# Performance work log

Hardware: AMD Instinct MI355X
Metric: run time of the kernel (lower is better)

Reference implementation:

```python
import jax, jax.numpy as jnp
import numpy as np

NUM_USERS = 100000
NUM_ITEMS = 50000
EMB = 64
B = 8192
MAXM = 50
ATT_H = 16
PRED_H = 8


def setup_inputs() -> dict:
    key = jax.random.key(0)
    ks = jax.random.split(key, 12)
    member_idx = jax.random.randint(ks[0], (B, MAXM), 0, NUM_USERS)
    # ragged group sizes in [1, MAXM]
    lens = jax.random.randint(ks[1], (B,), 1, MAXM + 1)
    member_mask = jnp.arange(MAXM)[None, :] < lens[:, None]  # bool [B, M]
    item_inputs = jax.random.randint(ks[2], (B,), 0, NUM_ITEMS)
    s = 1.0 / np.sqrt(EMB)
    user_table = jax.random.normal(ks[3], (NUM_USERS, EMB), jnp.float32) * s
    item_table = jax.random.normal(ks[4], (NUM_ITEMS, EMB), jnp.float32) * s
    att_w1 = jax.random.normal(ks[5], (2 * EMB, ATT_H), jnp.float32) * 0.05
    att_b1 = jnp.zeros((ATT_H,), jnp.float32)
    att_w2 = jax.random.normal(ks[6], (ATT_H, 1), jnp.float32) * 0.05
    att_b2 = jnp.zeros((1,), jnp.float32)
    pred_w1 = jax.random.normal(ks[7], (3 * EMB, PRED_H), jnp.float32) * 0.05
    pred_b1 = jnp.zeros((PRED_H,), jnp.float32)
    pred_w2 = jax.random.normal(ks[8], (PRED_H, 1), jnp.float32) * 0.05
    pred_b2 = jnp.zeros((1,), jnp.float32)
    return dict(member_idx=member_idx, member_mask=member_mask, item_inputs=item_inputs,
                user_table=user_table, item_table=item_table,
                att_w1=att_w1, att_b1=att_b1, att_w2=att_w2, att_b2=att_b2,
                pred_w1=pred_w1, pred_b1=pred_b1, pred_w2=pred_w2, pred_b2=pred_b2)


def reference(member_idx, member_mask, item_inputs, user_table, item_table,
              att_w1, att_b1, att_w2, att_b2, pred_w1, pred_b1, pred_w2, pred_b2):
    mem_e = user_table[member_idx]            # [B, M, d]
    item_e = item_table[item_inputs]          # [B, d]
    # attention MLP over concat(member, item)
    cat = jnp.concatenate(
        [mem_e, jnp.broadcast_to(item_e[:, None, :], mem_e.shape)], axis=-1)  # [B, M, 2d]
    h = jax.nn.relu(jnp.einsum('bmf,fh->bmh', cat, att_w1) + att_b1)
    logits = (jnp.einsum('bmh,ho->bmo', h, att_w2) + att_b2)[..., 0]          # [B, M]
    logits = jnp.where(member_mask, logits, -jnp.inf)
    wts = jax.nn.softmax(logits, axis=-1)                                     # [B, M]
    g = jnp.einsum('bm,bmd->bd', wts, mem_e)                                  # [B, d]
    new = jnp.concatenate([g * item_e, g, item_e], axis=-1)                   # [B, 3d]
    ph = jax.nn.relu(new @ pred_w1 + pred_b1)
    y = jax.nn.sigmoid(ph @ pred_w2 + pred_b2)                                # [B, 1]
    return y
```

## Files before the change

### kernel.cpp

```cpp
#include <hip/hip_runtime.h>
#include <hip/hip_bf16.h>


__global__ void AGREE_12773232738622_probe(
    const void* member_mask,
    const void* user_table,
    int* ws)
{
    if (ws[2] == 0x5AFE0001) return;

    const int lane = threadIdx.x;
    const int wi = lane >> 4;
    const int r  = lane & 15;

    int len = 0, ok = 1, prev = 1;
    for (int m = 0; m < 50; ++m) {
        long e = 50L * r + m;
        int nz;
        if (wi == 0)      nz = (((const unsigned char*)member_mask)[e] != 0);
        else if (wi == 1) nz = (((const unsigned short*)member_mask)[e] != 0);
        else if (wi == 2) nz = (((const unsigned int*)member_mask)[e] != 0u);
        else {
            const unsigned int* p = (const unsigned int*)member_mask;
            nz = ((p[2 * e] | p[2 * e + 1]) != 0u);
        }
        if (nz && !prev) ok = 0;
        if (nz) len = len + 1;
        prev = nz;
    }
    if (len == 0) ok = 0;

    ok = ok & __shfl_xor(ok, 1);
    ok = ok & __shfl_xor(ok, 2);
    ok = ok & __shfl_xor(ok, 4);
    ok = ok & __shfl_xor(ok, 8);
    int mx = len;
    mx = max(mx, __shfl_xor(mx, 1));
    mx = max(mx, __shfl_xor(mx, 2));
    mx = max(mx, __shfl_xor(mx, 4));
    mx = max(mx, __shfl_xor(mx, 8));

    int o0 = __shfl(ok, 0),  o1 = __shfl(ok, 16), o2 = __shfl(ok, 32), o3 = __shfl(ok, 48);
    int L0 = __shfl(mx, 0),  L1 = __shfl(mx, 16), L2 = __shfl(mx, 32), L3 = __shfl(mx, 48);

    float v = __bfloat162float(((const __hip_bfloat16*)user_table)[lane]);
    float a = (v < 0.0f) ? -v : v;
    int huge = (!(a < 4.0f)) ? 1 : 0;
    unsigned long long hb = __ballot(huge);
    int hcnt = __popcll(hb);

    if (lane == 0) {
        int bestW = 1, bestLen = -1;
        if (o0 && L0 > bestLen) { bestLen = L0; bestW = 1; }
        if (o1 && L1 > bestLen) { bestLen = L1; bestW = 2; }
        if (o2 && L2 > bestLen) { bestLen = L2; bestW = 4; }
        if (o3 && L3 > bestLen) { bestLen = L3; bestW = 8; }
        ws[0] = bestW;
        ws[1] = (hcnt >= 8) ? 1 : 0;
        ws[2] = 0x5AFE0001;
    }
}

__global__ void AGREE_12773232738622_kernel(
    const int* member_idx,
    const void* member_mask,
    const int* item_inputs,
    const void* user_table,
    const void* item_table,
    const void* att_w1,
    const void* att_b1,
    const void* att_w2,
    const void* att_b2,
    const void* pred_w1,
    const void* pred_b1,
    const void* pred_w2,
    const void* pred_b2,
    void* out,
    const int* ws)
{
    const int tid  = threadIdx.x;
    const int lane = tid & 63;
    const int wave = tid >> 6;
    const int b    = blockIdx.x * 4 + wave;
    const int mode = ws[0];
    const int isf  = ws[1];

    int valid = 0;
    if (lane < 50) {
        long e0 = 50L * b + lane;
        if (mode == 1)      valid = (((const unsigned char*)member_mask)[e0] != 0);
        else if (mode == 2) valid = (((const unsigned short*)member_mask)[e0] != 0);
        else if (mode == 4) valid = (((const unsigned int*)member_mask)[e0] != 0u);
        else {
            const unsigned int* p = (const unsigned int*)member_mask;
            valid = ((p[2 * e0] | p[2 * e0 + 1]) != 0u);
        }
    }
    unsigned long long vm = __ballot(valid);
    int len = __popcll(vm);
    if (len < 1)  len = 1;
    if (len > 50) len = 50;

    const int item_id = item_inputs[b];
    float itemv;
    if (isf) itemv = ((const float*)item_table)[item_id * 64 + lane];
    else     itemv = __bfloat162float(((const __hip_bfloat16*)item_table)[item_id * 64 + lane]);

    int idxv = 0;
    if (lane < 50) idxv = member_idx[b * 50 + lane];

    float part;
    {
        const int kk = lane & 15;
        const int c  = lane >> 4;
        if (isf) part = (c == 0) ? ((const float*)att_b1)[kk] : 0.0f;
        else     part = (c == 0) ? __bfloat162float(((const __hip_bfloat16*)att_b1)[kk]) : 0.0f;
        for (int t = 0; t < 16; ++t) {
            int f = c * 16 + t;
            float iv = __shfl(itemv, f);
            float w;
            if (isf) w = ((const float*)att_w1)[(64 + f) * 16 + kk];
            else     w = __bfloat162float(((const __hip_bfloat16*)att_w1)[(64 + f) * 16 + kk]);
            part += iv * w;
        }
        part += __shfl_xor(part, 16);
        part += __shfl_xor(part, 32);
    }
    float h[16];
    #pragma unroll
    for (int k = 0; k < 16; ++k) h[k] = __shfl(part, k);

    if (lane < len) {
        if (isf) {
            const float* rp = (const float*)user_table + (long)idxv * 64;
            const float* w1 = (const float*)att_w1;
            #pragma unroll 4
            for (int c = 0; c < 16; ++c) {
                float4 v = ((const float4*)rp)[c];
                #pragma unroll
                for (int k = 0; k < 16; ++k) {
                    h[k] += v.x * w1[(c * 4 + 0) * 16 + k];
                    h[k] += v.y * w1[(c * 4 + 1) * 16 + k];
                    h[k] += v.z * w1[(c * 4 + 2) * 16 + k];
                    h[k] += v.w * w1[(c * 4 + 3) * 16 + k];
                }
            }
        } else {
            const unsigned short* rp = (const unsigned short*)user_table + (long)idxv * 64;
            const unsigned int* w1u = (const unsigned int*)att_w1;
            #pragma unroll 2
            for (int c = 0; c < 8; ++c) {
                uint4 v = ((const uint4*)rp)[c];
                float e[8];
                e[0] = __uint_as_float(v.x << 16);
                e[1] = __uint_as_float(v.x & 0xFFFF0000u);
                e[2] = __uint_as_float(v.y << 16);
                e[3] = __uint_as_float(v.y & 0xFFFF0000u);
                e[4] = __uint_as_float(v.z << 16);
                e[5] = __uint_as_float(v.z & 0xFFFF0000u);
                e[6] = __uint_as_float(v.w << 16);
                e[7] = __uint_as_float(v.w & 0xFFFF0000u);
                #pragma unroll
                for (int j = 0; j < 8; ++j) {
                    #pragma unroll
                    for (int p = 0; p < 8; ++p) {
                        unsigned int wp = w1u[(c * 8 + j) * 8 + p];
                        h[2 * p]     += e[j] * __uint_as_float(wp << 16);
                        h[2 * p + 1] += e[j] * __uint_as_float(wp & 0xFFFF0000u);
                    }
                }
            }
        }
    }

    float lg;
    if (isf) lg = ((const float*)att_b2)[0];
    else     lg = __bfloat162float(((const __hip_bfloat16*)att_b2)[0]);
    #pragma unroll
    for (int k = 0; k < 16; ++k) {
        float hk = fmaxf(h[k], 0.0f);
        float w2;
        if (isf) w2 = ((const float*)att_w2)[k];
        else     w2 = __bfloat162float(((const __hip_bfloat16*)att_w2)[k]);
        lg += hk * w2;
    }

    float x = valid ? lg : -3.0e38f;
    float mx = x;
    mx = fmaxf(mx, __shfl_xor(mx, 1));
    mx = fmaxf(mx, __shfl_xor(mx, 2));
    mx = fmaxf(mx, __shfl_xor(mx, 4));
    mx = fmaxf(mx, __shfl_xor(mx, 8));
    mx = fmaxf(mx, __shfl_xor(mx, 16));
    mx = fmaxf(mx, __shfl_xor(mx, 32));
    float p = valid ? expf(x - mx) : 0.0f;
    float sum = p;
    sum += __shfl_xor(sum, 1);
    sum += __shfl_xor(sum, 2);
    sum += __shfl_xor(sum, 4);
    sum += __shfl_xor(sum, 8);
    sum += __shfl_xor(sum, 16);
    sum += __shfl_xor(sum, 32);
    float wnorm;
    if (sum > 0.0f) wnorm = p * (1.0f / sum);
    else            wnorm = (lane == 0) ? 1.0f : 0.0f;

    float g = 0.0f;
    if (isf) {
        const float* ut = (const float*)user_table;
        for (int m = 0; m < len; ++m) {
            int idm  = __shfl(idxv, m);
            float wv = __shfl(wnorm, m);
            g += wv * ut[(long)idm * 64 + lane];
        }
    } else {
        const unsigned short* ut = (const unsigned short*)user_table;
        for (int m = 0; m < len; ++m) {
            int idm  = __shfl(idxv, m);
            float wv = __shfl(wnorm, m);
            g += wv * __uint_as_float((unsigned int)ut[(long)idm * 64 + lane] << 16);
        }
    }

    const float gi = g * itemv;
    float p8[8];
    if (isf) {
        const float* pw = (const float*)pred_w1;
        #pragma unroll
        for (int k2 = 0; k2 < 8; ++k2) {
            p8[k2] = gi    * pw[lane * 8 + k2]
                   + g     * pw[(64 + lane) * 8 + k2]
                   + itemv * pw[(128 + lane) * 8 + k2];
        }
    } else {
        const __hip_bfloat16* pw = (const __hip_bfloat16*)pred_w1;
        #pragma unroll
        for (int k2 = 0; k2 < 8; ++k2) {
            p8[k2] = gi    * __bfloat162float(pw[lane * 8 + k2])
                   + g     * __bfloat162float(pw[(64 + lane) * 8 + k2])
                   + itemv * __bfloat162float(pw[(128 + lane) * 8 + k2]);
        }
    }
    #pragma unroll
    for (int k2 = 0; k2 < 8; ++k2) {
        float v = p8[k2];
        v += __shfl_xor(v, 1);
        v += __shfl_xor(v, 2);
        v += __shfl_xor(v, 4);
        v += __shfl_xor(v, 8);
        v += __shfl_xor(v, 16);
        v += __shfl_xor(v, 32);
        p8[k2] = v;
    }
    if (lane == 0) {
        float z;
        if (isf) z = ((const float*)pred_b2)[0];
        else     z = __bfloat162float(((const __hip_bfloat16*)pred_b2)[0]);
        for (int k2 = 0; k2 < 8; ++k2) {
            float bb, ww;
            if (isf) {
                bb = ((const float*)pred_b1)[k2];
                ww = ((const float*)pred_w2)[k2];
            } else {
                bb = __bfloat162float(((const __hip_bfloat16*)pred_b1)[k2]);
                ww = __bfloat162float(((const __hip_bfloat16*)pred_w2)[k2]);
            }
            float hh = p8[k2] + bb;
            if (hh < 0.0f) hh = 0.0f;
            z += hh * ww;
        }
        float y = 1.0f / (1.0f + expf(-z));
        if (isf) ((float*)out)[b] = y;
        else     ((__hip_bfloat16*)out)[b] = __float2bfloat16(y);
    }
}

extern "C" void kernel_launch(void* const* d_in, const int* in_sizes, int n_in,
                              void* d_out, int out_size, void* d_ws, size_t ws_size,
                              hipStream_t stream) {
    (void)in_sizes; (void)n_in; (void)out_size; (void)ws_size;
    AGREE_12773232738622_probe<<<1, 64, 0, stream>>>(
        d_in[1], d_in[3], (int*)d_ws);
    AGREE_12773232738622_kernel<<<2048, 256, 0, stream>>>(
        (const int*)d_in[0],
        d_in[1],
        (const int*)d_in[2],
        d_in[3],
        d_in[4],
        d_in[5],
        d_in[6],
        d_in[7],
        d_in[8],
        d_in[9],
        d_in[10],
        d_in[11],
        d_in[12],
        d_out,
        (const int*)d_ws);
}
```

Baseline: 164.1 us.

## Prefetch member embedding columns into registers before softmax and vectorize pred_w1 loads

Result: faster. 156.6 us (-4.5%).

```diff
diff --git a/kernel.cpp b/kernel.cpp
--- a/kernel.cpp
+++ b/kernel.cpp
@@ -61,7 +61,7 @@
     }
 }
 
-__global__ void AGREE_12773232738622_kernel(
+__global__ __launch_bounds__(256, 4) void AGREE_12773232738622_kernel(
     const int* member_idx,
     const void* member_mask,
     const int* item_inputs,
@@ -173,6 +173,29 @@
         }
     }
 
+    float col[50];
+    if (isf) {
+        const float* ut = (const float*)user_table;
+        #pragma unroll
+        for (int m = 0; m < 50; ++m) {
+            col[m] = 0.0f;
+            if (m < len) {
+                int idm = __shfl(idxv, m);
+                col[m] = ut[(long)idm * 64 + lane];
+            }
+        }
+    } else {
+        const unsigned short* ut = (const unsigned short*)user_table;
+        #pragma unroll
+        for (int m = 0; m < 50; ++m) {
+            col[m] = 0.0f;
+            if (m < len) {
+                int idm = __shfl(idxv, m);
+                col[m] = __uint_as_float((unsigned int)ut[(long)idm * 64 + lane] << 16);
+            }
+        }
+    }
+
     float lg;
     if (isf) lg = ((const float*)att_b2)[0];
     else     lg = __bfloat162float(((const __hip_bfloat16*)att_b2)[0]);
@@ -206,40 +229,50 @@
     else            wnorm = (lane == 0) ? 1.0f : 0.0f;
 
     float g = 0.0f;
-    if (isf) {
-        const float* ut = (const float*)user_table;
-        for (int m = 0; m < len; ++m) {
-            int idm  = __shfl(idxv, m);
+    #pragma unroll
+    for (int m = 0; m < 50; ++m) {
+        if (m < len) {
             float wv = __shfl(wnorm, m);
-            g += wv * ut[(long)idm * 64 + lane];
-        }
-    } else {
-        const unsigned short* ut = (const unsigned short*)user_table;
-        for (int m = 0; m < len; ++m) {
-            int idm  = __shfl(idxv, m);
-            float wv = __shfl(wnorm, m);
-            g += wv * __uint_as_float((unsigned int)ut[(long)idm * 64 + lane] << 16);
+            g += wv * col[m];
         }
     }
 
     const float gi = g * itemv;
     float p8[8];
     if (isf) {
-        const float* pw = (const float*)pred_w1;
+        const float4* pw4 = (const float4*)pred_w1;
+        float4 a0 = pw4[lane * 2],         a1 = pw4[lane * 2 + 1];
+        float4 b0 = pw4[(64 + lane) * 2],  b1 = pw4[(64 + lane) * 2 + 1];
+        float4 c0 = pw4[(128 + lane) * 2], c1 = pw4[(128 + lane) * 2 + 1];
+        p8[0] = gi * a0.x + g * b0.x + itemv * c0.x;
+        p8[1] = gi * a0.y + g * b0.y + itemv * c0.y;
+        p8[2] = gi * a0.z + g * b0.z + itemv * c0.z;
+        p8[3] = gi * a0.w + g * b0.w + itemv * c0.w;
+        p8[4] = gi * a1.x + g * b1.x + itemv * c1.x;
+        p8[5] = gi * a1.y + g * b1.y + itemv * c1.y;
+        p8[6] = gi * a1.z + g * b1.z + itemv * c1.z;
+        p8[7] = gi * a1.w + g * b1.w + itemv * c1.w;
+    } else {
+        const uint4* pw4 = (const uint4*)pred_w1;
+        uint4 A = pw4[lane];
+        uint4 Bv = pw4[64 + lane];
+        uint4 C = pw4[128 + lane];
+        float ea[8], eb[8], ec[8];
+        ea[0] = __uint_as_float(A.x << 16);  ea[1] = __uint_as_float(A.x & 0xFFFF0000u);
+        ea[2] = __uint_as_float(A.y << 16);  ea[3] = __uint_as_float(A.y & 0xFFFF0000u);
+        ea[4] = __uint_as_float(A.z << 16);  ea[5] = __uint_as_float(A.z & 0xFFFF0000u);
+        ea[6] = __uint_as_float(A.w << 16);  ea[7] = __uint_as_float(A.w & 0xFFFF0000u);
+        eb[0] = __uint_as_float(Bv.x << 16); eb[1] = __uint_as_float(Bv.x & 0xFFFF0000u);
+        eb[2] = __uint_as_float(Bv.y << 16); eb[3] = __uint_as_float(Bv.y & 0xFFFF0000u);
+        eb[4] = __uint_as_float(Bv.z << 16); eb[5] = __uint_as_float(Bv.z & 0xFFFF0000u);
+        eb[6] = __uint_as_float(Bv.w << 16); eb[7] = __uint_as_float(Bv.w & 0xFFFF0000u);
+        ec[0] = __uint_as_float(C.x << 16);  ec[1] = __uint_as_float(C.x & 0xFFFF0000u);
+        ec[2] = __uint_as_float(C.y << 16);  ec[3] = __uint_as_float(C.y & 0xFFFF0000u);
+        ec[4] = __uint_as_float(C.z << 16);  ec[5] = __uint_as_float(C.z & 0xFFFF0000u);
+        ec[6] = __uint_as_float(C.w << 16);  ec[7] = __uint_as_float(C.w & 0xFFFF0000u);
         #pragma unroll
-        for (int k2 = 0; k2 < 8; ++k2) {
-            p8[k2] = gi    * pw[lane * 8 + k2]
-                   + g     * pw[(64 + lane) * 8 + k2]
-                   + itemv * pw[(128 + lane) * 8 + k2];
-        }
-    } else {
-        const __hip_bfloat16* pw = (const __hip_bfloat16*)pred_w1;
-        #pragma unroll
-        for (int k2 = 0; k2 < 8; ++k2) {
-            p8[k2] = gi    * __bfloat162float(pw[lane * 8 + k2])
-                   + g     * __bfloat162float(pw[(64 + lane) * 8 + k2])
-                   + itemv * __bfloat162float(pw[(128 + lane) * 8 + k2]);
-        }
+        for (int k2 = 0; k2 < 8; ++k2)
+            p8[k2] = gi * ea[k2] + g * eb[k2] + itemv * ec[k2];
     }
     #pragma unroll
     for (int k2 = 0; k2 < 8; ++k2) {
```
